# Optimization experiments

Measured on AMD Instinct MI355X. Metric: run time of the kernel, lower is better.

The kernel has to match this reference:

```python
import jax, jax.numpy as jnp
import numpy as np

B, LT, LS, D, H, F = 4, 1024, 1024, 1024, 16, 4096
HD = D // H
EPS = 1e-6


def rms_norm(x, g):
    return x / jnp.sqrt(jnp.mean(x * x, axis=-1, keepdims=True) + EPS) * g


def mha(q_in, kv_in, wq, wk, wv, wo, bias):
    # q_in: [B,Lq,D], kv_in: [B,Lk,D], bias broadcastable to [B,H,Lq,Lk]
    b, lq, _ = q_in.shape
    lk = kv_in.shape[1]
    q = (q_in @ wq).reshape(b, lq, H, HD).transpose(0, 2, 1, 3)
    k = (kv_in @ wk).reshape(b, lk, H, HD).transpose(0, 2, 1, 3)
    v = (kv_in @ wv).reshape(b, lk, H, HD).transpose(0, 2, 1, 3)
    s = jnp.einsum('bhqd,bhkd->bhqk', q, k) / np.sqrt(HD).astype(np.float32) + bias
    o = jnp.einsum('bhqk,bhkd->bhqd', jax.nn.softmax(s, axis=-1), v)
    o = o.transpose(0, 2, 1, 3).reshape(b, lq, D) @ wo
    return o, k, v


def setup_inputs() -> dict:
    key = jax.random.key(0)
    ks = jax.random.split(key, 16)
    f = lambda k, sh, s: jax.random.normal(k, sh, jnp.float32) * s
    wscale = 1.0 / float(np.sqrt(D))
    causal = jnp.where(jnp.triu(jnp.ones((LT, LT), bool), 1), jnp.float32(-1e9), jnp.float32(0.0))
    return {
        'x': f(ks[0], (B, LT, D), 1.0),
        'memory': f(ks[1], (B, LS, D), 1.0),
        'position_embedding': f(ks[2], (1, H, LT, LS), 0.02),
        'causal_mask': causal,
        'gamma_sa': jnp.ones((D,), jnp.float32),
        'wq_s': f(ks[3], (D, D), wscale), 'wk_s': f(ks[4], (D, D), wscale),
        'wv_s': f(ks[5], (D, D), wscale), 'wo_s': f(ks[6], (D, D), wscale),
        'gamma_ca': jnp.ones((D,), jnp.float32),
        'wq_c': f(ks[7], (D, D), wscale), 'wk_c': f(ks[8], (D, D), wscale),
        'wv_c': f(ks[9], (D, D), wscale), 'wo_c': f(ks[10], (D, D), wscale),
        'gamma_m': jnp.ones((D,), jnp.float32),
        'w1': f(ks[11], (D, F), wscale), 'w2': f(ks[12], (F, D), 1.0 / float(np.sqrt(F))),
    }


def reference(x, memory, position_embedding, causal_mask,
              gamma_sa, wq_s, wk_s, wv_s, wo_s,
              gamma_ca, wq_c, wk_c, wv_c, wo_c,
              gamma_m, w1, w2):
    # self-attention block (pre-RMSNorm, causal mask, residual)
    h = rms_norm(x, gamma_sa)
    a, k_s, v_s = mha(h, h, wq_s, wk_s, wv_s, wo_s, causal_mask[None, None, :, :])
    attn_x = a + x
    # cross-attention block (position-embedding bias on scores, residual)
    h2 = rms_norm(attn_x, gamma_ca)
    c, k_c, v_c = mha(h2, memory, wq_c, wk_c, wv_c, wo_c, position_embedding)
    cross_x = c + attn_x
    # FFN block
    h3 = rms_norm(cross_x, gamma_m)
    mlp_x = jax.nn.relu(h3 @ w1) @ w2 + cross_x
    return mlp_x, (k_s, v_s), (k_c, v_c)
```

## Files before the change

kernel.cpp:

```cpp
#include <hip/hip_runtime.h>
#include <stdint.h>
#include <stddef.h>

typedef __bf16 bf16_t;
typedef __attribute__((ext_vector_type(8))) __bf16 bf16x8;
typedef __attribute__((ext_vector_type(4))) float f32x4;

#define LT 1024
#define LS 1024
#define DM 1024
#define NH 16
#define HD 64
#define FF 4096
#define BB 4

__device__ __forceinline__ void gld_lds16(const bf16_t* g, bf16_t* l) {
    __builtin_amdgcn_global_load_lds(
        (const __attribute__((address_space(1))) void*)g,
        (__attribute__((address_space(3))) void*)l, 16, 0, 0);
}

__global__ __launch_bounds__(256) void transpose_f2bf(
    const float* __restrict__ in, bf16_t* __restrict__ out, int R, int C)
{
    __shared__ float tile[32][33];
    int bx = blockIdx.x * 32;
    int by = blockIdx.y * 32;
    int tx = threadIdx.x, ty = threadIdx.y;
#pragma unroll
    for (int j = 0; j < 4; j++)
        tile[ty + j * 8][tx] = in[(size_t)(by + ty + j * 8) * C + bx + tx];
    __syncthreads();
#pragma unroll
    for (int j = 0; j < 4; j++)
        out[(size_t)(bx + ty + j * 8) * R + by + tx] = (bf16_t)tile[tx][ty + j * 8];
}

struct TPtrs { const float* in[8]; bf16_t* out[8]; };
__global__ __launch_bounds__(256) void transpose8_f2bf(TPtrs p)
{
    __shared__ float tile[32][33];
    const float* in = p.in[blockIdx.z];
    bf16_t* out = p.out[blockIdx.z];
    int bx = blockIdx.x * 32;
    int by = blockIdx.y * 32;
    int tx = threadIdx.x, ty = threadIdx.y;
#pragma unroll
    for (int j = 0; j < 4; j++)
        tile[ty + j * 8][tx] = in[(size_t)(by + ty + j * 8) * 1024 + bx + tx];
    __syncthreads();
#pragma unroll
    for (int j = 0; j < 4; j++)
        out[(size_t)(bx + ty + j * 8) * 1024 + by + tx] = (bf16_t)tile[tx][ty + j * 8];
}

__global__ __launch_bounds__(256) void transpose_bf(
    const bf16_t* __restrict__ in, bf16_t* __restrict__ out)
{
    __shared__ bf16_t tile[32][33];
    int bh = blockIdx.z;
    int r0 = blockIdx.x * 32;
    int c0 = blockIdx.y * 32;
    const bf16_t* ib = in + (size_t)bh * LT * HD;
    bf16_t* ob = out + (size_t)bh * HD * LT;
    int tx = threadIdx.x, ty = threadIdx.y;
#pragma unroll
    for (int j = 0; j < 4; j++)
        tile[ty + j * 8][tx] = ib[(size_t)(r0 + ty + j * 8) * HD + c0 + tx];
    __syncthreads();
#pragma unroll
    for (int j = 0; j < 4; j++)
        ob[(size_t)(c0 + ty + j * 8) * LT + r0 + tx] = tile[tx][ty + j * 8];
}

__global__ __launch_bounds__(256) void f2bf_kernel(
    const float* __restrict__ in, bf16_t* __restrict__ out, size_t n)
{
    size_t i = ((size_t)blockIdx.x * 256 + threadIdx.x) * 4;
    if (i + 3 < n) {
        float4 v = *(const float4*)&in[i];
        out[i + 0] = (bf16_t)v.x;
        out[i + 1] = (bf16_t)v.y;
        out[i + 2] = (bf16_t)v.z;
        out[i + 3] = (bf16_t)v.w;
    }
}

__global__ __launch_bounds__(256) void reduce2_res(
    const float* __restrict__ p, const float* __restrict__ res,
    float* __restrict__ out)
{
    const size_t MN = (size_t)BB * LT * DM;
    size_t i = ((size_t)blockIdx.x * 256 + threadIdx.x) * 4;
    float4 a = *(const float4*)&p[i];
    float4 b = *(const float4*)&p[i + MN];
    float4 r = *(const float4*)&res[i];
    float4 o;
    o.x = a.x + b.x + r.x; o.y = a.y + b.y + r.y;
    o.z = a.z + b.z + r.z; o.w = a.w + b.w + r.w;
    *(float4*)&out[i] = o;
}

__global__ __launch_bounds__(256) void rmsnorm_kernel(
    const float* __restrict__ x, const float* __restrict__ g,
    bf16_t* __restrict__ out)
{
    __shared__ float red[4];
    int row = blockIdx.x;
    int t = threadIdx.x;
    int lane = t & 63, w = t >> 6;
    const float* xr = x + (size_t)row * DM;
    float4 v = *(const float4*)&xr[t * 4];
    float ss = v.x * v.x + v.y * v.y + v.z * v.z + v.w * v.w;
#pragma unroll
    for (int off = 32; off > 0; off >>= 1) ss += __shfl_down(ss, off, 64);
    if (lane == 0) red[w] = ss;
    __syncthreads();
    float tot = red[0] + red[1] + red[2] + red[3];
    float inv = rsqrtf(tot * (1.0f / DM) + 1e-6f);
    float4 gv = *(const float4*)&g[t * 4];
    bf16_t* o = out + (size_t)row * DM + t * 4;
    o[0] = (bf16_t)(v.x * inv * gv.x);
    o[1] = (bf16_t)(v.y * inv * gv.y);
    o[2] = (bf16_t)(v.z * inv * gv.z);
    o[3] = (bf16_t)(v.w * inv * gv.w);
}

#define GEMM_BODY(Aptr, Btptr, Kstride, kBeg, kEnd)                              \
    for (int k0 = (kBeg); k0 < (kEnd); k0 += 64) {                               \
        __syncthreads();                                                         \
        _Pragma("unroll")                                                        \
        for (int i = 0; i < 4; i++) {                                            \
            int p = i * 256 + t;                                                 \
            int row = p >> 3;                                                    \
            int g = (p & 7) ^ (row & 7);                                         \
            gld_lds16(&(Aptr)[(size_t)(m0 + row) * (Kstride) + k0 + g * 8],      \
                      &lA[p * 8]);                                               \
            gld_lds16(&(Btptr)[(size_t)(n0 + row) * (Kstride) + k0 + g * 8],     \
                      &lB[p * 8]);                                               \
        }                                                                        \
        __syncthreads();                                                         \
        _Pragma("unroll")                                                        \
        for (int s = 0; s < 2; s++) {                                            \
            bf16x8 af[4], bfr[4];                                                \
            _Pragma("unroll")                                                    \
            for (int mt = 0; mt < 4; mt++) {                                     \
                int r = wr * 64 + mt * 16 + l15;                                 \
                af[mt] = *(const bf16x8*)&lA[((r << 3) + ((s * 4 + quad) ^ (r & 7))) << 3]; \
            }                                                                    \
            _Pragma("unroll")                                                    \
            for (int nt = 0; nt < 4; nt++) {                                     \
                int r = wc * 64 + nt * 16 + l15;                                 \
                bfr[nt] = *(const bf16x8*)&lB[((r << 3) + ((s * 4 + quad) ^ (r & 7))) << 3]; \
            }                                                                    \
            _Pragma("unroll")                                                    \
            for (int mt = 0; mt < 4; mt++)                                       \
                _Pragma("unroll")                                                \
                for (int nt = 0; nt < 4; nt++)                                   \
                    acc[mt][nt] = __builtin_amdgcn_mfma_f32_16x16x32_bf16(       \
                        af[mt], bfr[nt], acc[mt][nt], 0, 0, 0);                  \
        }                                                                        \
    }

__global__ __launch_bounds__(256) void gemm_qkv(
    const bf16_t* __restrict__ A1, const bf16_t* __restrict__ B1, int nb1,
    const bf16_t* __restrict__ A2, const bf16_t* __restrict__ B2, int secbase2,
    bf16_t* __restrict__ qb,
    float* __restrict__ kF, bf16_t* __restrict__ kB,
    float* __restrict__ vF, bf16_t* __restrict__ vB)
{
    __shared__ bf16_t lA[128 * 64];
    __shared__ bf16_t lB[128 * 64];
    const int t = threadIdx.x;
    const int lane = t & 63, w = t >> 6;
    const int quad = lane >> 4, l15 = lane & 15;
    const int m0 = blockIdx.x * 128;
    const int wr = w >> 1, wc = w & 1;

    const bf16_t* A; const bf16_t* Bt; int n0, sec0;
    if ((int)blockIdx.y < nb1) { A = A1; Bt = B1; n0 = blockIdx.y * 128; sec0 = 0; }
    else { A = A2; Bt = B2; n0 = (blockIdx.y - nb1) * 128; sec0 = secbase2; }

    f32x4 acc[4][4] = {};
    GEMM_BODY(A, Bt, 1024, 0, 1024)

#pragma unroll
    for (int mt = 0; mt < 4; mt++) {
#pragma unroll
        for (int nt = 0; nt < 4; nt++) {
#pragma unroll
            for (int r = 0; r < 4; r++) {
                int row = m0 + wr * 64 + mt * 16 + quad * 4 + r;
                int col = n0 + wc * 64 + nt * 16 + l15;
                float v = acc[mt][nt][r];
                int b = row >> 10, tp = row & 1023;
                int sec = sec0 + (col >> 10);
                int c10 = col & 1023;
                int h = c10 >> 6, d = c10 & 63;
                size_t idx = (((size_t)(b * NH + h)) << 16) + (size_t)tp * HD + d;
                if (sec == 0) {
                    qb[idx] = (bf16_t)v;
                } else if (sec == 1) {
                    kF[idx] = v;
                    kB[idx] = (bf16_t)v;
                } else {
                    vF[idx] = v;
                    vB[idx] = (bf16_t)v;
                }
            }
        }
    }
}

#define EP_RES 0
#define EP_RELU 1
#define EP_PART 2

template <int EP, int KSPLIT>
__global__ __launch_bounds__(256) void gemm_bt(
    const bf16_t* __restrict__ A, const bf16_t* __restrict__ Bt,
    int N, int K,
    float* __restrict__ outF, const float* __restrict__ res,
    bf16_t* __restrict__ outB)
{
    __shared__ bf16_t lA[128 * 64];
    __shared__ bf16_t lB[128 * 64];
    const int t = threadIdx.x;
    const int lane = t & 63, w = t >> 6;
    const int quad = lane >> 4, l15 = lane & 15;
    const int m0 = blockIdx.x * 128, n0 = blockIdx.y * 128;
    const int wr = w >> 1, wc = w & 1;
    const int Kc = K / KSPLIT;
    const int kBeg = blockIdx.z * Kc;

    f32x4 acc[4][4] = {};
    GEMM_BODY(A, Bt, K, kBeg, kBeg + Kc)

    float* dst = outF;
    if constexpr (EP == EP_PART)
        dst = outF + (size_t)blockIdx.z * (size_t)gridDim.x * 128 * N;

#pragma unroll
    for (int mt = 0; mt < 4; mt++) {
#pragma unroll
        for (int nt = 0; nt < 4; nt++) {
#pragma unroll
            for (int r = 0; r < 4; r++) {
                int row = m0 + wr * 64 + mt * 16 + quad * 4 + r;
                int col = n0 + wc * 64 + nt * 16 + l15;
                float v = acc[mt][nt][r];
                if constexpr (EP == EP_RES) {
                    dst[(size_t)row * N + col] = v + res[(size_t)row * N + col];
                } else if constexpr (EP == EP_RELU) {
                    outB[(size_t)row * N + col] = (bf16_t)fmaxf(v, 0.0f);
                } else {
                    dst[(size_t)row * N + col] = v;
                }
            }
        }
    }
}

template <bool CAUSAL>
__global__ __launch_bounds__(256, 4) void flash_attn(
    const bf16_t* __restrict__ Q, const bf16_t* __restrict__ Kb,
    const bf16_t* __restrict__ Vt, const float* __restrict__ bias,
    bf16_t* __restrict__ O)
{
    __shared__ bf16_t lK[2][64 * 64];
    __shared__ bf16_t lV[2][64 * 64];
    __shared__ bf16_t lP[4][16 * 64];
    const int t = threadIdx.x;
    const int lane = t & 63, w = t >> 6;
    const int quad = lane >> 4, l15 = lane & 15;
    const int qt = blockIdx.x;
    const int yy = blockIdx.y;
    const int h = yy >> 2, b = yy & 3;
    const int bhd = b * NH + h;
    const int q0 = qt * 64;

    const bf16_t* qbase = Q + (size_t)bhd * LT * HD;
    const bf16_t* kbase = Kb + (size_t)bhd * LS * HD;
    const bf16_t* vbase = Vt + (size_t)bhd * HD * LS;
    const float* bbase = bias + (size_t)h * LT * LS;

    bf16x8 qf[2];
    int qrow = q0 + w * 16 + l15;
#pragma unroll
    for (int s = 0; s < 2; s++)
        qf[s] = *(const bf16x8*)&qbase[(size_t)qrow * HD + s * 32 + quad * 8];

    f32x4 acc_o[4] = {};
    float m_i[4], l_i[4];
#pragma unroll
    for (int r = 0; r < 4; r++) { m_i[r] = -3.0e38f; l_i[r] = 0.0f; }

    const int nkt = CAUSAL ? (qt + 1) : (LS / 64);

#pragma unroll
    for (int i = 0; i < 2; i++) {
        int p = i * 256 + t;
        int row = p >> 3;
        int g = (p & 7) ^ (row & 7);
        gld_lds16(&kbase[(size_t)row * HD + g * 8], &lK[0][p * 8]);
        gld_lds16(&vbase[(size_t)row * LS + g * 8], &lV[0][p * 8]);
    }
    float bnxt[16], bcur[16];
    if constexpr (!CAUSAL) {
#pragma unroll
        for (int nt = 0; nt < 4; nt++)
#pragma unroll
            for (int r = 0; r < 4; r++)
                bnxt[nt * 4 + r] =
                    bbase[(size_t)(q0 + w * 16 + quad * 4 + r) * LS + nt * 16 + l15];
    }

    for (int kt = 0; kt < nkt; kt++) {
        const int d = kt & 1;
        const int nxt = kt + 1;
        if constexpr (!CAUSAL) {
#pragma unroll
            for (int i = 0; i < 16; i++) bcur[i] = bnxt[i];
        }
        if (nxt < nkt) {
            const int nb = nxt * 64;
            const int nd = nxt & 1;
#pragma unroll
            for (int i = 0; i < 2; i++) {
                int p = i * 256 + t;
                int row = p >> 3;
                int g = (p & 7) ^ (row & 7);
                gld_lds16(&kbase[(size_t)(nb + row) * HD + g * 8], &lK[nd][p * 8]);
                gld_lds16(&vbase[(size_t)row * LS + nb + g * 8], &lV[nd][p * 8]);
            }
            if constexpr (!CAUSAL) {
#pragma unroll
                for (int nt = 0; nt < 4; nt++)
#pragma unroll
                    for (int r = 0; r < 4; r++)
                        bnxt[nt * 4 + r] =
                            bbase[(size_t)(q0 + w * 16 + quad * 4 + r) * LS + nb + nt * 16 + l15];
                asm volatile("s_waitcnt vmcnt(20)" ::: "memory");
            } else {
                asm volatile("s_waitcnt vmcnt(4)" ::: "memory");
            }
        } else {
            asm volatile("s_waitcnt vmcnt(0)" ::: "memory");
        }
        __builtin_amdgcn_s_barrier();
        __builtin_amdgcn_sched_barrier(0);

        const int kb = kt * 64;
        f32x4 sacc[4];
#pragma unroll
        for (int nt = 0; nt < 4; nt++) {
            f32x4 sa = {};
#pragma unroll
            for (int s = 0; s < 2; s++) {
                int r = nt * 16 + l15;
                bf16x8 kf = *(const bf16x8*)&lK[d][((r << 3) + ((s * 4 + quad) ^ (r & 7))) << 3];
                sa = __builtin_amdgcn_mfma_f32_16x16x32_bf16(qf[s], kf, sa, 0, 0, 0);
            }
            sacc[nt] = sa;
        }

        float sval[4][4];
        float tmax[4];
#pragma unroll
        for (int r = 0; r < 4; r++) tmax[r] = -3.0e38f;
#pragma unroll
        for (int nt = 0; nt < 4; nt++) {
            int col = kb + nt * 16 + l15;
#pragma unroll
            for (int r = 0; r < 4; r++) {
                int row = q0 + w * 16 + quad * 4 + r;
                float v = sacc[nt][r] * 0.125f;
                if constexpr (CAUSAL) {
                    if (col > row) v = -1e9f;
                } else {
                    v += bcur[nt * 4 + r];
                }
                sval[nt][r] = v;
                tmax[r] = fmaxf(tmax[r], v);
            }
        }
#pragma unroll
        for (int r = 0; r < 4; r++) {
            float v = tmax[r];
            v = fmaxf(v, __shfl_xor(v, 1, 64));
            v = fmaxf(v, __shfl_xor(v, 2, 64));
            v = fmaxf(v, __shfl_xor(v, 4, 64));
            v = fmaxf(v, __shfl_xor(v, 8, 64));
            tmax[r] = v;
        }
        float alpha[4], rsum[4];
#pragma unroll
        for (int r = 0; r < 4; r++) {
            float mn = fmaxf(m_i[r], tmax[r]);
            alpha[r] = __expf(m_i[r] - mn);
            m_i[r] = mn;
            rsum[r] = 0.0f;
        }
#pragma unroll
        for (int nt = 0; nt < 4; nt++) {
#pragma unroll
            for (int r = 0; r < 4; r++) {
                float p = __expf(sval[nt][r] - m_i[r]);
                rsum[r] += p;
                int pr = quad * 4 + r;
                int gcol = nt * 2 + (l15 >> 3);
                lP[w][((pr << 3) + (gcol ^ (pr & 7))) * 8 + (l15 & 7)] = (bf16_t)p;
            }
        }
#pragma unroll
        for (int r = 0; r < 4; r++) {
            float v = rsum[r];
            v += __shfl_xor(v, 1, 64);
            v += __shfl_xor(v, 2, 64);
            v += __shfl_xor(v, 4, 64);
            v += __shfl_xor(v, 8, 64);
            l_i[r] = l_i[r] * alpha[r] + v;
        }
#pragma unroll
        for (int dt = 0; dt < 4; dt++)
#pragma unroll
            for (int r = 0; r < 4; r++)
                acc_o[dt][r] *= alpha[r];

#pragma unroll
        for (int s = 0; s < 2; s++) {
            bf16x8 pf = *(const bf16x8*)&lP[w][((l15 << 3) + ((s * 4 + quad) ^ (l15 & 7))) << 3];
#pragma unroll
            for (int dt = 0; dt < 4; dt++) {
                int r = dt * 16 + l15;
                bf16x8 vf = *(const bf16x8*)&lV[d][((r << 3) + ((s * 4 + quad) ^ (r & 7))) << 3];
                acc_o[dt] = __builtin_amdgcn_mfma_f32_16x16x32_bf16(pf, vf, acc_o[dt], 0, 0, 0);
            }
        }
        __builtin_amdgcn_s_barrier();
    }

#pragma unroll
    for (int dt = 0; dt < 4; dt++) {
#pragma unroll
        for (int r = 0; r < 4; r++) {
            int row = q0 + w * 16 + quad * 4 + r;
            int col = h * HD + dt * 16 + l15;
            float v = acc_o[dt][r] / l_i[r];
            O[((size_t)(b * LT + row)) * DM + col] = (bf16_t)v;
        }
    }
}

extern "C" void kernel_launch(void* const* d_in, const int* in_sizes, int n_in,
                              void* d_out, int out_size, void* d_ws, size_t ws_size,
                              hipStream_t stream)
{
    (void)in_sizes; (void)n_in; (void)out_size; (void)ws_size;
    const float* x    = (const float*)d_in[0];
    const float* mem  = (const float*)d_in[1];
    const float* pemb = (const float*)d_in[2];
    const float* g_sa = (const float*)d_in[4];
    const float* wq_s = (const float*)d_in[5];
    const float* wk_s = (const float*)d_in[6];
    const float* wv_s = (const float*)d_in[7];
    const float* wo_s = (const float*)d_in[8];
    const float* g_ca = (const float*)d_in[9];
    const float* wq_c = (const float*)d_in[10];
    const float* wk_c = (const float*)d_in[11];
    const float* wv_c = (const float*)d_in[12];
    const float* wo_c = (const float*)d_in[13];
    const float* g_m  = (const float*)d_in[14];
    const float* w1   = (const float*)d_in[15];
    const float* w2   = (const float*)d_in[16];
    float* out = (float*)d_out;

    const size_t OFF_KS = 4u * 1024 * 1024;
    const size_t OFF_VS = 8u * 1024 * 1024;
    const size_t OFF_KC = 12u * 1024 * 1024;
    const size_t OFF_VC = 16u * 1024 * 1024;

    char* ws = (char*)d_ws;
    const size_t MB = 1024 * 1024;
    bf16_t* wqkvTs = (bf16_t*)(ws + 0 * MB);
    bf16_t* woTs   = (bf16_t*)(ws + 6 * MB);
    bf16_t* wqTc   = (bf16_t*)(ws + 8 * MB);
    bf16_t* wkvTc  = (bf16_t*)(ws + 10 * MB);
    bf16_t* woTc   = (bf16_t*)(ws + 14 * MB);
    bf16_t* w1T    = (bf16_t*)(ws + 16 * MB);
    bf16_t* w2T    = (bf16_t*)(ws + 24 * MB);
    bf16_t* membf  = (bf16_t*)(ws + 32 * MB);
    bf16_t* hbuf   = (bf16_t*)(ws + 40 * MB);
    bf16_t* qbuf   = (bf16_t*)(ws + 48 * MB);
    bf16_t* kbuf   = (bf16_t*)(ws + 56 * MB);
    bf16_t* vbuf   = (bf16_t*)(ws + 64 * MB);
    bf16_t* vTbuf  = (bf16_t*)(ws + 72 * MB);
    bf16_t* Obuf   = (bf16_t*)(ws + 80 * MB);
    float*  attn_x  = (float*)(ws + 88 * MB);
    float*  cross_x = (float*)(ws + 112 * MB);
    bf16_t* ffnmid  = (bf16_t*)(ws + 48 * MB);
    float*  part    = (float*)(ws + 80 * MB);

    dim3 tb(32, 8);
    TPtrs tp;
    tp.in[0] = wq_s; tp.out[0] = wqkvTs;
    tp.in[1] = wk_s; tp.out[1] = wqkvTs + 1024 * 1024;
    tp.in[2] = wv_s; tp.out[2] = wqkvTs + 2 * 1024 * 1024;
    tp.in[3] = wo_s; tp.out[3] = woTs;
    tp.in[4] = wq_c; tp.out[4] = wqTc;
    tp.in[5] = wk_c; tp.out[5] = wkvTc;
    tp.in[6] = wv_c; tp.out[6] = wkvTc + 1024 * 1024;
    tp.in[7] = wo_c; tp.out[7] = woTc;
    transpose8_f2bf<<<dim3(32, 32, 8), tb, 0, stream>>>(tp);
    transpose_f2bf<<<dim3(128, 32), tb, 0, stream>>>(w1, w1T, DM, FF);
    transpose_f2bf<<<dim3(32, 128), tb, 0, stream>>>(w2, w2T, FF, DM);

    f2bf_kernel<<<4096, 256, 0, stream>>>(mem, membf, (size_t)BB * LS * DM);

    rmsnorm_kernel<<<BB * LT, 256, 0, stream>>>(x, g_sa, hbuf);
    gemm_qkv<<<dim3(32, 24), 256, 0, stream>>>(
        hbuf, wqkvTs, 24, hbuf, wqkvTs, 0,
        qbuf, out + OFF_KS, kbuf, out + OFF_VS, vbuf);
    transpose_bf<<<dim3(32, 2, 64), tb, 0, stream>>>(vbuf, vTbuf);
    flash_attn<true><<<dim3(16, 64), 256, 0, stream>>>(qbuf, kbuf, vTbuf, nullptr, Obuf);
    gemm_bt<EP_RES, 1><<<dim3(32, 8), 256, 0, stream>>>(
        Obuf, woTs, 1024, 1024, attn_x, x, nullptr);

    rmsnorm_kernel<<<BB * LT, 256, 0, stream>>>(attn_x, g_ca, hbuf);
    gemm_qkv<<<dim3(32, 24), 256, 0, stream>>>(
        hbuf, wqTc, 8, membf, wkvTc, 1,
        qbuf, out + OFF_KC, kbuf, out + OFF_VC, vbuf);
    transpose_bf<<<dim3(32, 2, 64), tb, 0, stream>>>(vbuf, vTbuf);
    flash_attn<false><<<dim3(16, 64), 256, 0, stream>>>(qbuf, kbuf, vTbuf, pemb, Obuf);
    gemm_bt<EP_RES, 1><<<dim3(32, 8), 256, 0, stream>>>(
        Obuf, woTc, 1024, 1024, cross_x, attn_x, nullptr);

    rmsnorm_kernel<<<BB * LT, 256, 0, stream>>>(cross_x, g_m, hbuf);
    gemm_bt<EP_RELU, 1><<<dim3(32, 32), 256, 0, stream>>>(
        hbuf, w1T, 4096, 1024, nullptr, nullptr, ffnmid);
    gemm_bt<EP_PART, 2><<<dim3(32, 8, 2), 256, 0, stream>>>(
        ffnmid, w2T, 1024, 4096, part, nullptr, nullptr);
    reduce2_res<<<4096, 256, 0, stream>>>(part, cross_x, out);
}
```

Before: 618.7 us.

## Transpose QK^T MFMA layout, use lazy softmax rescaling and packed P stores

The QK^T MFMA operands are swapped so each lane holds scores for a single query row. Row max and sum reductions then shrink to two cross-quad shuffles, and the per-row state collapses to scalars. The online-softmax rescale of the output accumulator is skipped unless some row's max grows by more than a threshold, P is written to LDS as packed 4-wide bf16 stores, and bias loads are reordered and use the new layout. s_setprio is added around the MFMA loops. The lazy rescaling relies on bounded exponent growth and adds a wave-wide vote plus shuffles to broadcast alpha and l back into the output layout.

After: 600.3 us. -3.0%, faster.

```diff
diff --git a/kernel.cpp b/kernel.cpp
--- a/kernel.cpp
+++ b/kernel.cpp
@@ -4,6 +4,7 @@
 
 typedef __bf16 bf16_t;
 typedef __attribute__((ext_vector_type(8))) __bf16 bf16x8;
+typedef __attribute__((ext_vector_type(4))) __bf16 bf16x4;
 typedef __attribute__((ext_vector_type(4))) float f32x4;
 
 #define LT 1024
@@ -285,18 +286,25 @@
     const float* bbase = bias + (size_t)h * LT * LS;
 
     bf16x8 qf[2];
-    int qrow = q0 + w * 16 + l15;
+    const int qrow = q0 + w * 16 + l15;
 #pragma unroll
     for (int s = 0; s < 2; s++)
         qf[s] = *(const bf16x8*)&qbase[(size_t)qrow * HD + s * 32 + quad * 8];
 
     f32x4 acc_o[4] = {};
-    float m_i[4], l_i[4];
-#pragma unroll
-    for (int r = 0; r < 4; r++) { m_i[r] = -3.0e38f; l_i[r] = 0.0f; }
+    float m_i = -3.0e38f, l_i = 0.0f;
 
     const int nkt = CAUSAL ? (qt + 1) : (LS / 64);
 
+    float bnxt[16], bcur[16];
+    if constexpr (!CAUSAL) {
+#pragma unroll
+        for (int nt = 0; nt < 4; nt++)
+#pragma unroll
+            for (int r = 0; r < 4; r++)
+                bnxt[nt * 4 + r] =
+                    bbase[(size_t)qrow * LS + nt * 16 + quad * 4 + r];
+    }
 #pragma unroll
     for (int i = 0; i < 2; i++) {
         int p = i * 256 + t;
@@ -305,15 +313,6 @@
         gld_lds16(&kbase[(size_t)row * HD + g * 8], &lK[0][p * 8]);
         gld_lds16(&vbase[(size_t)row * LS + g * 8], &lV[0][p * 8]);
     }
-    float bnxt[16], bcur[16];
-    if constexpr (!CAUSAL) {
-#pragma unroll
-        for (int nt = 0; nt < 4; nt++)
-#pragma unroll
-            for (int r = 0; r < 4; r++)
-                bnxt[nt * 4 + r] =
-                    bbase[(size_t)(q0 + w * 16 + quad * 4 + r) * LS + nt * 16 + l15];
-    }
 
     for (int kt = 0; kt < nkt; kt++) {
         const int d = kt & 1;
@@ -325,6 +324,14 @@
         if (nxt < nkt) {
             const int nb = nxt * 64;
             const int nd = nxt & 1;
+            if constexpr (!CAUSAL) {
+#pragma unroll
+                for (int nt = 0; nt < 4; nt++)
+#pragma unroll
+                    for (int r = 0; r < 4; r++)
+                        bnxt[nt * 4 + r] =
+                            bbase[(size_t)qrow * LS + nb + nt * 16 + quad * 4 + r];
+            }
 #pragma unroll
             for (int i = 0; i < 2; i++) {
                 int p = i * 256 + t;
@@ -334,12 +341,6 @@
                 gld_lds16(&vbase[(size_t)row * LS + nb + g * 8], &lV[nd][p * 8]);
             }
             if constexpr (!CAUSAL) {
-#pragma unroll
-                for (int nt = 0; nt < 4; nt++)
-#pragma unroll
-                    for (int r = 0; r < 4; r++)
-                        bnxt[nt * 4 + r] =
-                            bbase[(size_t)(q0 + w * 16 + quad * 4 + r) * LS + nb + nt * 16 + l15];
                 asm volatile("s_waitcnt vmcnt(20)" ::: "memory");
             } else {
                 asm volatile("s_waitcnt vmcnt(4)" ::: "memory");
@@ -351,7 +352,9 @@
         __builtin_amdgcn_sched_barrier(0);
 
         const int kb = kt * 64;
+
         f32x4 sacc[4];
+        __builtin_amdgcn_s_setprio(1);
 #pragma unroll
         for (int nt = 0; nt < 4; nt++) {
             f32x4 sa = {};
@@ -359,94 +362,93 @@
             for (int s = 0; s < 2; s++) {
                 int r = nt * 16 + l15;
                 bf16x8 kf = *(const bf16x8*)&lK[d][((r << 3) + ((s * 4 + quad) ^ (r & 7))) << 3];
-                sa = __builtin_amdgcn_mfma_f32_16x16x32_bf16(qf[s], kf, sa, 0, 0, 0);
+                sa = __builtin_amdgcn_mfma_f32_16x16x32_bf16(kf, qf[s], sa, 0, 0, 0);
             }
             sacc[nt] = sa;
         }
+        __builtin_amdgcn_s_setprio(0);
 
         float sval[4][4];
-        float tmax[4];
-#pragma unroll
-        for (int r = 0; r < 4; r++) tmax[r] = -3.0e38f;
+        float tmn[4];
 #pragma unroll
         for (int nt = 0; nt < 4; nt++) {
-            int col = kb + nt * 16 + l15;
 #pragma unroll
             for (int r = 0; r < 4; r++) {
-                int row = q0 + w * 16 + quad * 4 + r;
                 float v = sacc[nt][r] * 0.125f;
                 if constexpr (CAUSAL) {
-                    if (col > row) v = -1e9f;
+                    int col = kb + nt * 16 + quad * 4 + r;
+                    if (col > qrow) v = -1e9f;
                 } else {
                     v += bcur[nt * 4 + r];
                 }
                 sval[nt][r] = v;
-                tmax[r] = fmaxf(tmax[r], v);
-            }
-        }
-#pragma unroll
-        for (int r = 0; r < 4; r++) {
-            float v = tmax[r];
-            v = fmaxf(v, __shfl_xor(v, 1, 64));
-            v = fmaxf(v, __shfl_xor(v, 2, 64));
-            v = fmaxf(v, __shfl_xor(v, 4, 64));
-            v = fmaxf(v, __shfl_xor(v, 8, 64));
-            tmax[r] = v;
-        }
-        float alpha[4], rsum[4];
-#pragma unroll
-        for (int r = 0; r < 4; r++) {
-            float mn = fmaxf(m_i[r], tmax[r]);
-            alpha[r] = __expf(m_i[r] - mn);
-            m_i[r] = mn;
-            rsum[r] = 0.0f;
-        }
+            }
+            tmn[nt] = fmaxf(fmaxf(sval[nt][0], sval[nt][1]),
+                            fmaxf(sval[nt][2], sval[nt][3]));
+        }
+        float tm = fmaxf(fmaxf(tmn[0], tmn[1]), fmaxf(tmn[2], tmn[3]));
+        tm = fmaxf(tm, __shfl_xor(tm, 16, 64));
+        tm = fmaxf(tm, __shfl_xor(tm, 32, 64));
+
+        if (!__all(tm <= m_i + 8.0f)) {
+            float mn = fmaxf(m_i, tm);
+            float alpha = __expf(m_i - mn);
+            m_i = mn;
+            l_i *= alpha;
+            float ar[4];
+#pragma unroll
+            for (int r = 0; r < 4; r++) ar[r] = __shfl(alpha, quad * 4 + r, 64);
+#pragma unroll
+            for (int dt = 0; dt < 4; dt++)
+#pragma unroll
+                for (int r = 0; r < 4; r++) acc_o[dt][r] *= ar[r];
+        }
+
+        float rs[4];
 #pragma unroll
         for (int nt = 0; nt < 4; nt++) {
-#pragma unroll
-            for (int r = 0; r < 4; r++) {
-                float p = __expf(sval[nt][r] - m_i[r]);
-                rsum[r] += p;
-                int pr = quad * 4 + r;
-                int gcol = nt * 2 + (l15 >> 3);
-                lP[w][((pr << 3) + (gcol ^ (pr & 7))) * 8 + (l15 & 7)] = (bf16_t)p;
-            }
-        }
-#pragma unroll
-        for (int r = 0; r < 4; r++) {
-            float v = rsum[r];
-            v += __shfl_xor(v, 1, 64);
-            v += __shfl_xor(v, 2, 64);
-            v += __shfl_xor(v, 4, 64);
-            v += __shfl_xor(v, 8, 64);
-            l_i[r] = l_i[r] * alpha[r] + v;
-        }
-#pragma unroll
-        for (int dt = 0; dt < 4; dt++)
-#pragma unroll
-            for (int r = 0; r < 4; r++)
-                acc_o[dt][r] *= alpha[r];
+            float p0 = __expf(sval[nt][0] - m_i);
+            float p1 = __expf(sval[nt][1] - m_i);
+            float p2 = __expf(sval[nt][2] - m_i);
+            float p3 = __expf(sval[nt][3] - m_i);
+            rs[nt] = (p0 + p1) + (p2 + p3);
+            bf16x4 pk;
+            pk[0] = (bf16_t)p0; pk[1] = (bf16_t)p1;
+            pk[2] = (bf16_t)p2; pk[3] = (bf16_t)p3;
+            int gc = nt * 2 + (quad >> 1);
+            int eoff = ((l15 << 3) + (gc ^ (l15 & 7))) * 8 + (quad & 1) * 4;
+            *(bf16x4*)&lP[w][eoff] = pk;
+        }
+        float rsum = (rs[0] + rs[1]) + (rs[2] + rs[3]);
+        rsum += __shfl_xor(rsum, 16, 64);
+        rsum += __shfl_xor(rsum, 32, 64);
+        l_i += rsum;
 
 #pragma unroll
         for (int s = 0; s < 2; s++) {
             bf16x8 pf = *(const bf16x8*)&lP[w][((l15 << 3) + ((s * 4 + quad) ^ (l15 & 7))) << 3];
+            __builtin_amdgcn_s_setprio(1);
 #pragma unroll
             for (int dt = 0; dt < 4; dt++) {
                 int r = dt * 16 + l15;
                 bf16x8 vf = *(const bf16x8*)&lV[d][((r << 3) + ((s * 4 + quad) ^ (r & 7))) << 3];
                 acc_o[dt] = __builtin_amdgcn_mfma_f32_16x16x32_bf16(pf, vf, acc_o[dt], 0, 0, 0);
             }
+            __builtin_amdgcn_s_setprio(0);
         }
         __builtin_amdgcn_s_barrier();
     }
 
+    float lr[4];
+#pragma unroll
+    for (int r = 0; r < 4; r++) lr[r] = __shfl(l_i, quad * 4 + r, 64);
 #pragma unroll
     for (int dt = 0; dt < 4; dt++) {
 #pragma unroll
         for (int r = 0; r < 4; r++) {
             int row = q0 + w * 16 + quad * 4 + r;
             int col = h * HD + dt * 16 + l15;
-            float v = acc_o[dt][r] / l_i[r];
+            float v = acc_o[dt][r] / lr[r];
             O[((size_t)(b * LT + row)) * DM + col] = (bf16_t)v;
         }
     }
```
